# Kernel optimization log

Measured on AMD Instinct MI355X. Metric: run time of the kernel, lower is better.

The kernel has to match this reference:

```python
import jax, jax.numpy as jnp
import numpy as np

N, F, H, L, O, E = 20000, 128, 128, 4, 64, 640000
NEG_SLOPE = 0.2  # PyG GATConv default


def setup_inputs() -> dict:
    key = jax.random.key(0)
    ks = jax.random.split(key, 8)
    x = jax.random.normal(ks[0], (N, F), dtype=jnp.float32)
    edge_index = jax.random.randint(ks[1], (2, E), 0, N, dtype=jnp.int64)
    sc = 1.0 / np.sqrt(F)
    Ws = jax.random.normal(ks[2], (L, F, H), dtype=jnp.float32) * sc
    att_src = jax.random.normal(ks[3], (L, H), dtype=jnp.float32) * sc
    att_dst = jax.random.normal(ks[4], (L, H), dtype=jnp.float32) * sc
    biases = jnp.zeros((L, H), dtype=jnp.float32)
    W_out = jax.random.normal(ks[5], (H, O), dtype=jnp.float32) * (1.0 / np.sqrt(H))
    b_out = jnp.zeros((O,), dtype=jnp.float32)
    return {"x": x, "edge_index": edge_index, "Ws": Ws, "att_src": att_src,
            "att_dst": att_dst, "biases": biases, "W_out": W_out, "b_out": b_out}


def _gat_conv(h, src, dst, W, a_s, a_d, b):
    # h: [N, F_in]; single-head GATConv (PyG semantics)
    z = h @ W                                   # [N, H]
    alpha_s = z @ a_s                           # [N]
    alpha_d = z @ a_d                           # [N]
    logits = jax.nn.leaky_relu(alpha_s[src] + alpha_d[dst], negative_slope=NEG_SLOPE)  # [E']
    # segment-softmax over edges grouped by destination node
    m = jax.ops.segment_max(logits, dst, num_segments=N)
    p = jnp.exp(logits - m[dst])
    s = jax.ops.segment_sum(p, dst, num_segments=N)
    alpha = p / (s[dst] + 1e-16)                # [E']
    out = jax.ops.segment_sum(alpha[:, None] * z[src], dst, num_segments=N)  # [N, H]
    return out + b


def reference(x, edge_index, Ws, att_src, att_dst, biases, W_out, b_out):
    # add self-loops once (PyG GATConv default add_self_loops=True)
    loop = jnp.arange(N, dtype=edge_index.dtype)
    src = jnp.concatenate([edge_index[0], loop])
    dst = jnp.concatenate([edge_index[1], loop])
    h = x
    for l in range(L):
        h = _gat_conv(h, src, dst, Ws[l], att_src[l], att_dst[l], biases[l])
        h = jax.nn.relu(h)  # Dropout is identity at eval
    return h @ W_out + b_out  # [N, O]
```

## Files before the change

### kernel.cpp

```cpp
#include <hip/hip_runtime.h>

#define NN 20000
#define FF 128
#define HH 128
#define LL 4
#define OO 64
#define EE 640000
#define NEG 0.2f
#define NB ((NN + 255) / 256)
#define NTILES (NN / 16)

typedef short bf16x8 __attribute__((ext_vector_type(8)));
typedef float f32x4 __attribute__((ext_vector_type(4)));

__device__ inline ushort f2bf(float f) {
    uint u = __float_as_uint(f);
    return (ushort)((u + 0x7fffu + ((u >> 16) & 1u)) >> 16);
}


__global__ void k_init_counters(int* __restrict__ counters) {
    int i = blockIdx.x * 256 + threadIdx.x;
    if (i < NN) counters[i] = 1;
}

__global__ void k_hist(const int* __restrict__ dst, int* __restrict__ counters) {
    int e = blockIdx.x * 256 + threadIdx.x;
    if (e < EE) atomicAdd(&counters[dst[e]], 1);
}

__global__ void k_partial(const int* __restrict__ counters, int* __restrict__ partials) {
    __shared__ int ws[4];
    int t = threadIdx.x;
    int i = blockIdx.x * 256 + t;
    int c = (i < NN) ? counters[i] : 0;
    #pragma unroll
    for (int off = 32; off; off >>= 1) c += __shfl_xor(c, off);
    if ((t & 63) == 0) ws[t >> 6] = c;
    __syncthreads();
    if (t == 0) partials[blockIdx.x] = ws[0] + ws[1] + ws[2] + ws[3];
}

__global__ void k_scan_small(const int* __restrict__ partials, int* __restrict__ offsets) {
    __shared__ int sp[128];
    int t = threadIdx.x;
    int v = (t < NB) ? partials[t] : 0;
    sp[t] = v;
    __syncthreads();
    for (int off = 1; off < 128; off <<= 1) {
        int u = (t >= off) ? sp[t - off] : 0;
        __syncthreads();
        sp[t] += u;
        __syncthreads();
    }
    if (t < NB) offsets[t] = sp[t] - v;
}

__global__ void k_apply(const int* __restrict__ counters, const int* __restrict__ offsets,
                        int* __restrict__ row_off, int* __restrict__ cursor,
                        int* __restrict__ src_sorted) {
    __shared__ int sc[256];
    int t = threadIdx.x;
    int i = blockIdx.x * 256 + t;
    int c = (i < NN) ? counters[i] : 0;
    sc[t] = c;
    __syncthreads();
    for (int off = 1; off < 256; off <<= 1) {
        int u = (t >= off) ? sc[t - off] : 0;
        __syncthreads();
        sc[t] += u;
        __syncthreads();
    }
    int incl = sc[t];
    int base = offsets[blockIdx.x];
    if (i < NN) {
        int excl = base + incl - c;
        row_off[i] = excl;
        cursor[i] = excl + 1;
        src_sorted[excl] = i;
        if (i == NN - 1) row_off[NN] = base + incl;
    }
}

__global__ void k_scatter(const int* __restrict__ src, const int* __restrict__ dst,
                          int* __restrict__ cursor, int* __restrict__ src_sorted) {
    int e = blockIdx.x * 256 + threadIdx.x;
    if (e < EE) {
        int p = atomicAdd(&cursor[dst[e]], 1);
        src_sorted[p] = src[e];
    }
}


__global__ void k_convw(const float* __restrict__ Ws, const float* __restrict__ Wout,
                        ushort* __restrict__ wh, ushort* __restrict__ wl) {
    int idx = blockIdx.x * 256 + threadIdx.x;
    const int per_l = HH * 128;
    float v;
    if (idx < LL * per_l) {
        int l = idx / per_l, rem = idx % per_l;
        int n = rem >> 7, k = rem & 127;
        v = Ws[(size_t)l * 128 * HH + (size_t)k * HH + n];
    } else {
        int j = idx - LL * per_l;
        if (j >= OO * 128) return;
        int n = j >> 7, k = j & 127;
        v = Wout[(size_t)k * OO + n];
    }
    ushort h = f2bf(v);
    float hf = __uint_as_float((uint)h << 16);
    wh[idx] = h;
    wl[idx] = f2bf(v - hf);
}


__global__ void k_wa(const float* __restrict__ Ws, const float* __restrict__ attS,
                     const float* __restrict__ attD, float* __restrict__ wa) {
    int t = blockIdx.x * 256 + threadIdx.x;
    if (t >= LL * 256) return;
    int l = t >> 8, rem = t & 255, which = rem >> 7, k = rem & 127;
    const float* wrow = Ws + (size_t)l * 128 * HH + (size_t)k * HH;
    const float* av = (which ? attD : attS) + l * HH;
    float s = 0.f;
    #pragma unroll 4
    for (int n = 0; n < HH; n++) s += wrow[n] * av[n];
    wa[l * 256 + which * 128 + k] = s;
}


__device__ inline void do_agg(const float* __restrict__ z, const float* __restrict__ as,
                              const float* __restrict__ ad, const int* __restrict__ row_off,
                              const int* __restrict__ srcs, const float* __restrict__ bias,
                              float (*h)[132], int node0, int wid, int l64) {
    int g = l64 >> 5, cl = l64 & 31;
    const float4* zb = (const float4*)z;
    #pragma unroll 1
    for (int i = 0; i < 4; i++) {
        int node = node0 + wid * 4 + i;
        int beg = row_off[node], end = row_off[node + 1];
        float adn = ad[node];
        float lself = as[node] + adn;
        float mx = (lself >= 0.f) ? lself : NEG * lself;

        float4 acc = make_float4(0.f, 0.f, 0.f, 0.f);
        float s = 0.f;
        for (int e = beg + g; e < end; e += 16) {
            int e1 = e + 2, e2 = e + 4, e3 = e + 6, e4 = e + 8, e5 = e + 10, e6 = e + 12, e7 = e + 14;
            int lim = end - 1;
            int i1 = min(e1, lim), i2 = min(e2, lim), i3 = min(e3, lim);
            int i4 = min(e4, lim), i5 = min(e5, lim), i6 = min(e6, lim), i7 = min(e7, lim);
            int s0 = srcs[e], s1 = srcs[i1], s2 = srcs[i2], s3 = srcs[i3];
            int s4 = srcs[i4], s5 = srcs[i5], s6 = srcs[i6], s7 = srcs[i7];
            float l0 = as[s0] + adn, l1 = as[s1] + adn, l2 = as[s2] + adn, l3 = as[s3] + adn;
            float l4 = as[s4] + adn, l5 = as[s5] + adn, l6 = as[s6] + adn, l7 = as[s7] + adn;
            l0 = (l0 >= 0.f) ? l0 : NEG * l0;  l1 = (l1 >= 0.f) ? l1 : NEG * l1;
            l2 = (l2 >= 0.f) ? l2 : NEG * l2;  l3 = (l3 >= 0.f) ? l3 : NEG * l3;
            l4 = (l4 >= 0.f) ? l4 : NEG * l4;  l5 = (l5 >= 0.f) ? l5 : NEG * l5;
            l6 = (l6 >= 0.f) ? l6 : NEG * l6;  l7 = (l7 >= 0.f) ? l7 : NEG * l7;
            float4 z0 = zb[(size_t)s0 * 32 + cl];
            float4 z1 = zb[(size_t)s1 * 32 + cl];
            float4 z2 = zb[(size_t)s2 * 32 + cl];
            float4 z3 = zb[(size_t)s3 * 32 + cl];
            float4 z4 = zb[(size_t)s4 * 32 + cl];
            float4 z5 = zb[(size_t)s5 * 32 + cl];
            float4 z6 = zb[(size_t)s6 * 32 + cl];
            float4 z7 = zb[(size_t)s7 * 32 + cl];
            float p0 = __expf(l0 - mx);
            float p1 = (e1 < end) ? __expf(l1 - mx) : 0.f;
            float p2 = (e2 < end) ? __expf(l2 - mx) : 0.f;
            float p3 = (e3 < end) ? __expf(l3 - mx) : 0.f;
            float p4 = (e4 < end) ? __expf(l4 - mx) : 0.f;
            float p5 = (e5 < end) ? __expf(l5 - mx) : 0.f;
            float p6 = (e6 < end) ? __expf(l6 - mx) : 0.f;
            float p7 = (e7 < end) ? __expf(l7 - mx) : 0.f;
            s += ((p0 + p1) + (p2 + p3)) + ((p4 + p5) + (p6 + p7));
            acc.x += (p0 * z0.x + p1 * z1.x + p2 * z2.x + p3 * z3.x)
                   + (p4 * z4.x + p5 * z5.x + p6 * z6.x + p7 * z7.x);
            acc.y += (p0 * z0.y + p1 * z1.y + p2 * z2.y + p3 * z3.y)
                   + (p4 * z4.y + p5 * z5.y + p6 * z6.y + p7 * z7.y);
            acc.z += (p0 * z0.z + p1 * z1.z + p2 * z2.z + p3 * z3.z)
                   + (p4 * z4.z + p5 * z5.z + p6 * z6.z + p7 * z7.z);
            acc.w += (p0 * z0.w + p1 * z1.w + p2 * z2.w + p3 * z3.w)
                   + (p4 * z4.w + p5 * z5.w + p6 * z6.w + p7 * z7.w);
        }
        acc.x += __shfl_xor(acc.x, 32);
        acc.y += __shfl_xor(acc.y, 32);
        acc.z += __shfl_xor(acc.z, 32);
        acc.w += __shfl_xor(acc.w, 32);
        s     += __shfl_xor(s, 32);
        if (g == 0) {
            float inv = 1.f / (s + 1e-16f);
            float4 b = ((const float4*)bias)[cl];
            int lrow = wid * 4 + i;
            h[lrow][cl * 4 + 0] = fmaxf(acc.x * inv + b.x, 0.f);
            h[lrow][cl * 4 + 1] = fmaxf(acc.y * inv + b.y, 0.f);
            h[lrow][cl * 4 + 2] = fmaxf(acc.z * inv + b.z, 0.f);
            h[lrow][cl * 4 + 3] = fmaxf(acc.w * inv + b.w, 0.f);
        }
    }
}

template <int NCOL, bool BIAS, bool ALPHAS>
__device__ inline void do_gemm(const float (*h)[132], const ushort* __restrict__ wh,
                               const ushort* __restrict__ wl, const float* __restrict__ bias,
                               float* __restrict__ C, const float* __restrict__ wa,
                               float* __restrict__ as_o, float* __restrict__ ad_o,
                               int row0, int wid, int l64) {
    constexpr int CT = NCOL / 32;
    if (CT < 4 && wid >= CT) return;
    int ct = wid;
    int lr = l64 & 15, lg = l64 >> 4;
    int col0 = ct * 32;

    f32x4 af0[4], af1[4];
    #pragma unroll
    for (int s = 0; s < 4; s++) {
        af0[s] = *(const f32x4*)&h[lr][s * 32 + lg * 8];
        af1[s] = *(const f32x4*)&h[lr][s * 32 + lg * 8 + 4];
    }
    bf16x8 ah[4], al[4];
    #pragma unroll
    for (int s = 0; s < 4; s++) {
        #pragma unroll
        for (int j = 0; j < 8; j++) {
            float v = (j < 4) ? af0[s][j] : af1[s][j - 4];
            ushort hb = f2bf(v);
            float hf = __uint_as_float((uint)hb << 16);
            ah[s][j] = (short)hb;
            al[s][j] = (short)f2bf(v - hf);
        }
    }

    f32x4 acc[2] = {{0.f, 0.f, 0.f, 0.f}, {0.f, 0.f, 0.f, 0.f}};
    #pragma unroll
    for (int s = 0; s < 4; s++) {
        #pragma unroll
        for (int nt = 0; nt < 2; nt++) {
            int woff = (col0 + nt * 16 + lr) * 128 + s * 32 + lg * 8;
            bf16x8 bh = *(const bf16x8*)(wh + woff);
            bf16x8 bl = *(const bf16x8*)(wl + woff);
            acc[nt] = __builtin_amdgcn_mfma_f32_16x16x32_bf16(ah[s], bh, acc[nt], 0, 0, 0);
            acc[nt] = __builtin_amdgcn_mfma_f32_16x16x32_bf16(ah[s], bl, acc[nt], 0, 0, 0);
            acc[nt] = __builtin_amdgcn_mfma_f32_16x16x32_bf16(al[s], bh, acc[nt], 0, 0, 0);
        }
    }

    int orow = lg * 4;
    #pragma unroll
    for (int nt = 0; nt < 2; nt++) {
        #pragma unroll
        for (int r = 0; r < 4; r++) {
            float v = acc[nt][r];
            if (BIAS) v += bias[col0 + nt * 16 + lr];
            C[(size_t)(row0 + orow + r) * NCOL + col0 + nt * 16 + lr] = v;
        }
    }

    if constexpr (ALPHAS) {
        if (ct == 0) {
            float ps = 0.f, pd = 0.f;
            #pragma unroll
            for (int s = 0; s < 4; s++) {
                #pragma unroll
                for (int j = 0; j < 8; j++) {
                    float v = (j < 4) ? af0[s][j] : af1[s][j - 4];
                    int k = s * 32 + lg * 8 + j;
                    ps += v * wa[k];
                    pd += v * wa[128 + k];
                }
            }
            ps += __shfl_xor(ps, 16);  pd += __shfl_xor(pd, 16);
            ps += __shfl_xor(ps, 32);  pd += __shfl_xor(pd, 32);
            if (lg == 0) {
                as_o[row0 + lr] = ps;
                ad_o[row0 + lr] = pd;
            }
        }
    }
}


__global__ __launch_bounds__(256)
void k_layer0(const float* __restrict__ x, const ushort* __restrict__ wh,
              const ushort* __restrict__ wl, const float* __restrict__ wa,
              float* __restrict__ z, float* __restrict__ as_o, float* __restrict__ ad_o) {
    __shared__ float h[16][132];
    int t = threadIdx.x, wid = t >> 6, l64 = t & 63;
    int row0 = blockIdx.x * 16;
    for (int i = t; i < 16 * 32; i += 256) {
        int r = i >> 5, c4 = (i & 31) << 2;
        *(float4*)&h[r][c4] = *(const float4*)&x[(size_t)(row0 + r) * 128 + c4];
    }
    __syncthreads();
    do_gemm<HH, false, true>(h, wh, wl, nullptr, z, wa, as_o, ad_o, row0, wid, l64);
}

template <int NCOL, bool BIAS, bool ALPHAS>
__global__ __launch_bounds__(256)
void k_layer(const float* __restrict__ zin, const float* __restrict__ asi,
             const float* __restrict__ adi, const int* __restrict__ row_off,
             const int* __restrict__ srcs, const float* __restrict__ abias,
             const ushort* __restrict__ wh, const ushort* __restrict__ wl,
             const float* __restrict__ cbias, const float* __restrict__ wa,
             float* __restrict__ zout, float* __restrict__ as_o, float* __restrict__ ad_o) {
    __shared__ float h[16][132];
    int t = threadIdx.x, wid = t >> 6, l64 = t & 63;
    int row0 = blockIdx.x * 16;
    do_agg(zin, asi, adi, row_off, srcs, abias, h, row0, wid, l64);
    __syncthreads();
    do_gemm<NCOL, BIAS, ALPHAS>(h, wh, wl, cbias, zout, wa, as_o, ad_o, row0, wid, l64);
}


extern "C" void kernel_launch(void* const* d_in, const int* in_sizes, int n_in,
                              void* d_out, int out_size, void* d_ws, size_t ws_size,
                              hipStream_t stream) {
    const float* x      = (const float*)d_in[0];
    const int*   ei     = (const int*)d_in[1];
    const float* Ws     = (const float*)d_in[2];
    const float* attS   = (const float*)d_in[3];
    const float* attD   = (const float*)d_in[4];
    const float* biases = (const float*)d_in[5];
    const float* W_out  = (const float*)d_in[6];
    const float* b_out  = (const float*)d_in[7];
    float* out = (float*)d_out;

    const int* srcp = ei;
    const int* dstp = ei + EE;

    char* w = (char*)d_ws;
    auto take = [&](size_t bytes) {
        char* p = w;
        w += (bytes + 15) & ~(size_t)15;
        return p;
    };
    float*  za         = (float*)take((size_t)NN * HH * 4);
    float*  zbv        = (float*)take((size_t)NN * HH * 4);
    float*  asa        = (float*)take((size_t)NN * 4);
    float*  ada        = (float*)take((size_t)NN * 4);
    float*  asb        = (float*)take((size_t)NN * 4);
    float*  adb        = (float*)take((size_t)NN * 4);
    int*    counters   = (int*)take((size_t)NN * 4);
    int*    row_off    = (int*)take((size_t)(NN + 1) * 4);
    int*    cursor     = (int*)take((size_t)NN * 4);
    int*    src_sorted = (int*)take((size_t)(EE + NN) * 4);
    int*    partials   = (int*)take((size_t)NB * 4);
    int*    offsets    = (int*)take((size_t)NB * 4);
    const int WTOT = LL * HH * 128 + OO * 128;
    ushort* whbuf      = (ushort*)take((size_t)WTOT * 2);
    ushort* wlbuf      = (ushort*)take((size_t)WTOT * 2);
    float*  wabuf      = (float*)take((size_t)LL * 256 * 4);

    k_init_counters<<<(NN + 255) / 256, 256, 0, stream>>>(counters);
    k_hist<<<(EE + 255) / 256, 256, 0, stream>>>(dstp, counters);
    k_partial<<<NB, 256, 0, stream>>>(counters, partials);
    k_scan_small<<<1, 128, 0, stream>>>(partials, offsets);
    k_apply<<<NB, 256, 0, stream>>>(counters, offsets, row_off, cursor, src_sorted);
    k_scatter<<<(EE + 255) / 256, 256, 0, stream>>>(srcp, dstp, cursor, src_sorted);
    k_convw<<<(WTOT + 255) / 256, 256, 0, stream>>>(Ws, W_out, whbuf, wlbuf);
    k_wa<<<(LL * 256 + 255) / 256, 256, 0, stream>>>(Ws, attS, attD, wabuf);

    k_layer0<<<NTILES, 256, 0, stream>>>(x, whbuf, wlbuf, wabuf, za, asa, ada);

    k_layer<HH, false, true><<<NTILES, 256, 0, stream>>>(
        za, asa, ada, row_off, src_sorted, biases + 0 * HH,
        whbuf + (size_t)1 * HH * 128, wlbuf + (size_t)1 * HH * 128,
        nullptr, wabuf + 1 * 256, zbv, asb, adb);
    k_layer<HH, false, true><<<NTILES, 256, 0, stream>>>(
        zbv, asb, adb, row_off, src_sorted, biases + 1 * HH,
        whbuf + (size_t)2 * HH * 128, wlbuf + (size_t)2 * HH * 128,
        nullptr, wabuf + 2 * 256, za, asa, ada);
    k_layer<HH, false, true><<<NTILES, 256, 0, stream>>>(
        za, asa, ada, row_off, src_sorted, biases + 2 * HH,
        whbuf + (size_t)3 * HH * 128, wlbuf + (size_t)3 * HH * 128,
        nullptr, wabuf + 3 * 256, zbv, asb, adb);

    k_layer<OO, true, false><<<NTILES, 256, 0, stream>>>(
        zbv, asb, adb, row_off, src_sorted, biases + 3 * HH,
        whbuf + (size_t)LL * HH * 128, wlbuf + (size_t)LL * HH * 128,
        b_out, nullptr, out, nullptr, nullptr);
}
```

Measured before the change: 377.2 us.

## Pack attention scalars into padded z rows and double threads per block

Stores alpha_src and alpha_dst in the first two floats of each node's z row, padded to a 132-float stride with features at offset 4. This lets the gather read the logit scalar from the same row as the feature vector instead of from separate arrays. Blocks grow to 512 threads: each wave aggregates 2 nodes instead of 4, and the GEMM gives each wave one 16-column tile instead of two. The padding makes the z buffers slightly larger, and the scalar at offset 0 may sit in a different cache line from the features, so the locality gain is not assured.

```diff
diff --git a/kernel.cpp b/kernel.cpp
--- a/kernel.cpp
+++ b/kernel.cpp
@@ -9,6 +9,7 @@
 #define NEG 0.2f
 #define NB ((NN + 255) / 256)
 #define NTILES (NN / 16)
+#define ZS 132
 
 typedef short bf16x8 __attribute__((ext_vector_type(8)));
 typedef float f32x4 __attribute__((ext_vector_type(4)));
@@ -128,18 +129,17 @@
 }
 
 
-__device__ inline void do_agg(const float* __restrict__ z, const float* __restrict__ as,
-                              const float* __restrict__ ad, const int* __restrict__ row_off,
+__device__ inline void do_agg(const float* __restrict__ zin, const int* __restrict__ row_off,
                               const int* __restrict__ srcs, const float* __restrict__ bias,
                               float (*h)[132], int node0, int wid, int l64) {
     int g = l64 >> 5, cl = l64 & 31;
-    const float4* zb = (const float4*)z;
+    const float4* zb = (const float4*)zin;
     #pragma unroll 1
-    for (int i = 0; i < 4; i++) {
-        int node = node0 + wid * 4 + i;
+    for (int i = 0; i < 2; i++) {
+        int node = node0 + wid * 2 + i;
         int beg = row_off[node], end = row_off[node + 1];
-        float adn = ad[node];
-        float lself = as[node] + adn;
+        float adn = zin[(size_t)node * ZS + 1];
+        float lself = zin[(size_t)node * ZS] + adn;
         float mx = (lself >= 0.f) ? lself : NEG * lself;
 
         float4 acc = make_float4(0.f, 0.f, 0.f, 0.f);
@@ -151,20 +151,22 @@
             int i4 = min(e4, lim), i5 = min(e5, lim), i6 = min(e6, lim), i7 = min(e7, lim);
             int s0 = srcs[e], s1 = srcs[i1], s2 = srcs[i2], s3 = srcs[i3];
             int s4 = srcs[i4], s5 = srcs[i5], s6 = srcs[i6], s7 = srcs[i7];
-            float l0 = as[s0] + adn, l1 = as[s1] + adn, l2 = as[s2] + adn, l3 = as[s3] + adn;
-            float l4 = as[s4] + adn, l5 = as[s5] + adn, l6 = as[s6] + adn, l7 = as[s7] + adn;
+            float l0 = zin[(size_t)s0 * ZS] + adn, l1 = zin[(size_t)s1 * ZS] + adn;
+            float l2 = zin[(size_t)s2 * ZS] + adn, l3 = zin[(size_t)s3 * ZS] + adn;
+            float l4 = zin[(size_t)s4 * ZS] + adn, l5 = zin[(size_t)s5 * ZS] + adn;
+            float l6 = zin[(size_t)s6 * ZS] + adn, l7 = zin[(size_t)s7 * ZS] + adn;
             l0 = (l0 >= 0.f) ? l0 : NEG * l0;  l1 = (l1 >= 0.f) ? l1 : NEG * l1;
             l2 = (l2 >= 0.f) ? l2 : NEG * l2;  l3 = (l3 >= 0.f) ? l3 : NEG * l3;
             l4 = (l4 >= 0.f) ? l4 : NEG * l4;  l5 = (l5 >= 0.f) ? l5 : NEG * l5;
             l6 = (l6 >= 0.f) ? l6 : NEG * l6;  l7 = (l7 >= 0.f) ? l7 : NEG * l7;
-            float4 z0 = zb[(size_t)s0 * 32 + cl];
-            float4 z1 = zb[(size_t)s1 * 32 + cl];
-            float4 z2 = zb[(size_t)s2 * 32 + cl];
-            float4 z3 = zb[(size_t)s3 * 32 + cl];
-            float4 z4 = zb[(size_t)s4 * 32 + cl];
-            float4 z5 = zb[(size_t)s5 * 32 + cl];
-            float4 z6 = zb[(size_t)s6 * 32 + cl];
-            float4 z7 = zb[(size_t)s7 * 32 + cl];
+            float4 z0 = zb[(size_t)s0 * 33 + 1 + cl];
+            float4 z1 = zb[(size_t)s1 * 33 + 1 + cl];
+            float4 z2 = zb[(size_t)s2 * 33 + 1 + cl];
+            float4 z3 = zb[(size_t)s3 * 33 + 1 + cl];
+            float4 z4 = zb[(size_t)s4 * 33 + 1 + cl];
+            float4 z5 = zb[(size_t)s5 * 33 + 1 + cl];
+            float4 z6 = zb[(size_t)s6 * 33 + 1 + cl];
+            float4 z7 = zb[(size_t)s7 * 33 + 1 + cl];
             float p0 = __expf(l0 - mx);
             float p1 = (e1 < end) ? __expf(l1 - mx) : 0.f;
             float p2 = (e2 < end) ? __expf(l2 - mx) : 0.f;
@@ -191,7 +193,7 @@
         if (g == 0) {
             float inv = 1.f / (s + 1e-16f);
             float4 b = ((const float4*)bias)[cl];
-            int lrow = wid * 4 + i;
+            int lrow = wid * 2 + i;
             h[lrow][cl * 4 + 0] = fmaxf(acc.x * inv + b.x, 0.f);
             h[lrow][cl * 4 + 1] = fmaxf(acc.y * inv + b.y, 0.f);
             h[lrow][cl * 4 + 2] = fmaxf(acc.z * inv + b.z, 0.f);
@@ -200,17 +202,15 @@
     }
 }
 
-template <int NCOL, bool BIAS, bool ALPHAS>
+template <int NCOL, bool BIAS, bool ALPHAS, bool PACKED>
 __device__ inline void do_gemm(const float (*h)[132], const ushort* __restrict__ wh,
                                const ushort* __restrict__ wl, const float* __restrict__ bias,
                                float* __restrict__ C, const float* __restrict__ wa,
-                               float* __restrict__ as_o, float* __restrict__ ad_o,
                                int row0, int wid, int l64) {
-    constexpr int CT = NCOL / 32;
-    if (CT < 4 && wid >= CT) return;
-    int ct = wid;
+    constexpr int CT = NCOL / 16;
+    if (wid >= CT) return;
     int lr = l64 & 15, lg = l64 >> 4;
-    int col0 = ct * 32;
+    int col0 = wid * 16;
 
     f32x4 af0[4], af1[4];
     #pragma unroll
@@ -231,33 +231,30 @@
         }
     }
 
-    f32x4 acc[2] = {{0.f, 0.f, 0.f, 0.f}, {0.f, 0.f, 0.f, 0.f}};
+    f32x4 acc = {0.f, 0.f, 0.f, 0.f};
     #pragma unroll
     for (int s = 0; s < 4; s++) {
-        #pragma unroll
-        for (int nt = 0; nt < 2; nt++) {
-            int woff = (col0 + nt * 16 + lr) * 128 + s * 32 + lg * 8;
-            bf16x8 bh = *(const bf16x8*)(wh + woff);
-            bf16x8 bl = *(const bf16x8*)(wl + woff);
-            acc[nt] = __builtin_amdgcn_mfma_f32_16x16x32_bf16(ah[s], bh, acc[nt], 0, 0, 0);
-            acc[nt] = __builtin_amdgcn_mfma_f32_16x16x32_bf16(ah[s], bl, acc[nt], 0, 0, 0);
-            acc[nt] = __builtin_amdgcn_mfma_f32_16x16x32_bf16(al[s], bh, acc[nt], 0, 0, 0);
-        }
+        int woff = (col0 + lr) * 128 + s * 32 + lg * 8;
+        bf16x8 bh = *(const bf16x8*)(wh + woff);
+        bf16x8 bl = *(const bf16x8*)(wl + woff);
+        acc = __builtin_amdgcn_mfma_f32_16x16x32_bf16(ah[s], bh, acc, 0, 0, 0);
+        acc = __builtin_amdgcn_mfma_f32_16x16x32_bf16(ah[s], bl, acc, 0, 0, 0);
+        acc = __builtin_amdgcn_mfma_f32_16x16x32_bf16(al[s], bh, acc, 0, 0, 0);
     }
 
     int orow = lg * 4;
     #pragma unroll
-    for (int nt = 0; nt < 2; nt++) {
-        #pragma unroll
-        for (int r = 0; r < 4; r++) {
-            float v = acc[nt][r];
-            if (BIAS) v += bias[col0 + nt * 16 + lr];
-            C[(size_t)(row0 + orow + r) * NCOL + col0 + nt * 16 + lr] = v;
-        }
+    for (int r = 0; r < 4; r++) {
+        float v = acc[r];
+        if (BIAS) v += bias[col0 + lr];
+        if (PACKED)
+            C[(size_t)(row0 + orow + r) * ZS + 4 + col0 + lr] = v;
+        else
+            C[(size_t)(row0 + orow + r) * NCOL + col0 + lr] = v;
     }
 
     if constexpr (ALPHAS) {
-        if (ct == 0) {
+        if (wid == 0) {
             float ps = 0.f, pd = 0.f;
             #pragma unroll
             for (int s = 0; s < 4; s++) {
@@ -272,43 +269,42 @@
             ps += __shfl_xor(ps, 16);  pd += __shfl_xor(pd, 16);
             ps += __shfl_xor(ps, 32);  pd += __shfl_xor(pd, 32);
             if (lg == 0) {
-                as_o[row0 + lr] = ps;
-                ad_o[row0 + lr] = pd;
+                C[(size_t)(row0 + lr) * ZS + 0] = ps;
+                C[(size_t)(row0 + lr) * ZS + 1] = pd;
             }
         }
     }
 }
 
 
-__global__ __launch_bounds__(256)
+__global__ __launch_bounds__(512)
 void k_layer0(const float* __restrict__ x, const ushort* __restrict__ wh,
               const ushort* __restrict__ wl, const float* __restrict__ wa,
-              float* __restrict__ z, float* __restrict__ as_o, float* __restrict__ ad_o) {
+              float* __restrict__ z) {
     __shared__ float h[16][132];
     int t = threadIdx.x, wid = t >> 6, l64 = t & 63;
     int row0 = blockIdx.x * 16;
-    for (int i = t; i < 16 * 32; i += 256) {
-        int r = i >> 5, c4 = (i & 31) << 2;
+    {
+        int r = t >> 5, c4 = (t & 31) << 2;
         *(float4*)&h[r][c4] = *(const float4*)&x[(size_t)(row0 + r) * 128 + c4];
     }
     __syncthreads();
-    do_gemm<HH, false, true>(h, wh, wl, nullptr, z, wa, as_o, ad_o, row0, wid, l64);
-}
-
-template <int NCOL, bool BIAS, bool ALPHAS>
-__global__ __launch_bounds__(256)
-void k_layer(const float* __restrict__ zin, const float* __restrict__ asi,
-             const float* __restrict__ adi, const int* __restrict__ row_off,
+    do_gemm<HH, false, true, true>(h, wh, wl, nullptr, z, wa, row0, wid, l64);
+}
+
+template <int NCOL, bool BIAS, bool ALPHAS, bool PACKED>
+__global__ __launch_bounds__(512)
+void k_layer(const float* __restrict__ zin, const int* __restrict__ row_off,
              const int* __restrict__ srcs, const float* __restrict__ abias,
              const ushort* __restrict__ wh, const ushort* __restrict__ wl,
              const float* __restrict__ cbias, const float* __restrict__ wa,
-             float* __restrict__ zout, float* __restrict__ as_o, float* __restrict__ ad_o) {
+             float* __restrict__ zout) {
     __shared__ float h[16][132];
     int t = threadIdx.x, wid = t >> 6, l64 = t & 63;
     int row0 = blockIdx.x * 16;
-    do_agg(zin, asi, adi, row_off, srcs, abias, h, row0, wid, l64);
-    __syncthreads();
-    do_gemm<NCOL, BIAS, ALPHAS>(h, wh, wl, cbias, zout, wa, as_o, ad_o, row0, wid, l64);
+    do_agg(zin, row_off, srcs, abias, h, row0, wid, l64);
+    __syncthreads();
+    do_gemm<NCOL, BIAS, ALPHAS, PACKED>(h, wh, wl, cbias, zout, wa, row0, wid, l64);
 }
 
 
@@ -334,12 +330,8 @@
         w += (bytes + 15) & ~(size_t)15;
         return p;
     };
-    float*  za         = (float*)take((size_t)NN * HH * 4);
-    float*  zbv        = (float*)take((size_t)NN * HH * 4);
-    float*  asa        = (float*)take((size_t)NN * 4);
-    float*  ada        = (float*)take((size_t)NN * 4);
-    float*  asb        = (float*)take((size_t)NN * 4);
-    float*  adb        = (float*)take((size_t)NN * 4);
+    float*  za         = (float*)take((size_t)NN * ZS * 4);
+    float*  zbv        = (float*)take((size_t)NN * ZS * 4);
     int*    counters   = (int*)take((size_t)NN * 4);
     int*    row_off    = (int*)take((size_t)(NN + 1) * 4);
     int*    cursor     = (int*)take((size_t)NN * 4);
@@ -360,23 +352,23 @@
     k_convw<<<(WTOT + 255) / 256, 256, 0, stream>>>(Ws, W_out, whbuf, wlbuf);
     k_wa<<<(LL * 256 + 255) / 256, 256, 0, stream>>>(Ws, attS, attD, wabuf);
 
-    k_layer0<<<NTILES, 256, 0, stream>>>(x, whbuf, wlbuf, wabuf, za, asa, ada);
-
-    k_layer<HH, false, true><<<NTILES, 256, 0, stream>>>(
-        za, asa, ada, row_off, src_sorted, biases + 0 * HH,
+    k_layer0<<<NTILES, 512, 0, stream>>>(x, whbuf, wlbuf, wabuf, za);
+
+    k_layer<HH, false, true, true><<<NTILES, 512, 0, stream>>>(
+        za, row_off, src_sorted, biases + 0 * HH,
         whbuf + (size_t)1 * HH * 128, wlbuf + (size_t)1 * HH * 128,
-        nullptr, wabuf + 1 * 256, zbv, asb, adb);
-    k_layer<HH, false, true><<<NTILES, 256, 0, stream>>>(
-        zbv, asb, adb, row_off, src_sorted, biases + 1 * HH,
+        nullptr, wabuf + 1 * 256, zbv);
+    k_layer<HH, false, true, true><<<NTILES, 512, 0, stream>>>(
+        zbv, row_off, src_sorted, biases + 1 * HH,
         whbuf + (size_t)2 * HH * 128, wlbuf + (size_t)2 * HH * 128,
-        nullptr, wabuf + 2 * 256, za, asa, ada);
-    k_layer<HH, false, true><<<NTILES, 256, 0, stream>>>(
-        za, asa, ada, row_off, src_sorted, biases + 2 * HH,
+        nullptr, wabuf + 2 * 256, za);
+    k_layer<HH, false, true, true><<<NTILES, 512, 0, stream>>>(
+        za, row_off, src_sorted, biases + 2 * HH,
         whbuf + (size_t)3 * HH * 128, wlbuf + (size_t)3 * HH * 128,
-        nullptr, wabuf + 3 * 256, zbv, asb, adb);
-
-    k_layer<OO, true, false><<<NTILES, 256, 0, stream>>>(
-        zbv, asb, adb, row_off, src_sorted, biases + 3 * HH,
+        nullptr, wabuf + 3 * 256, zbv);
+
+    k_layer<OO, true, false, false><<<NTILES, 512, 0, stream>>>(
+        zbv, row_off, src_sorted, biases + 3 * HH,
         whbuf + (size_t)LL * HH * 128, wlbuf + (size_t)LL * HH * 128,
-        b_out, nullptr, out, nullptr, nullptr);
-}
+        b_out, nullptr, out);
+}
```

Result: faster. 361.0 us (-4.3%).

## Use one wavefront per node in fused GAT layers with larger blocks

Applied to the files above, without the earlier changes.

Each 16-node tile block now launches 16 wavefronts (1024 threads), with each wave aggregating a single destination node instead of four nodes serially. The GEMM stage splits output columns into 16-wide slices, one per wave, so up to 8 waves do MFMA work instead of 4. Layer 0 uses 512 threads so each thread loads exactly one float4 of the input tile. The aim is more memory-level parallelism for the gather-heavy aggregation. The cost is larger blocks, a register cap of 1024 threads per block, and idle waves during the GEMM phase.

```diff
diff --git a/kernel.cpp b/kernel.cpp
--- a/kernel.cpp
+++ b/kernel.cpp
@@ -128,77 +128,73 @@
 }
 
 
-__device__ inline void do_agg(const float* __restrict__ z, const float* __restrict__ as,
-                              const float* __restrict__ ad, const int* __restrict__ row_off,
-                              const int* __restrict__ srcs, const float* __restrict__ bias,
-                              float (*h)[132], int node0, int wid, int l64) {
+__device__ inline void do_agg1(const float* __restrict__ z, const float* __restrict__ asv,
+                               const float* __restrict__ adv, const int* __restrict__ row_off,
+                               const int* __restrict__ srcs, const float* __restrict__ bias,
+                               float (*h)[132], int node, int lrow, int l64) {
     int g = l64 >> 5, cl = l64 & 31;
     const float4* zb = (const float4*)z;
-    #pragma unroll 1
-    for (int i = 0; i < 4; i++) {
-        int node = node0 + wid * 4 + i;
-        int beg = row_off[node], end = row_off[node + 1];
-        float adn = ad[node];
-        float lself = as[node] + adn;
-        float mx = (lself >= 0.f) ? lself : NEG * lself;
-
-        float4 acc = make_float4(0.f, 0.f, 0.f, 0.f);
-        float s = 0.f;
-        for (int e = beg + g; e < end; e += 16) {
-            int e1 = e + 2, e2 = e + 4, e3 = e + 6, e4 = e + 8, e5 = e + 10, e6 = e + 12, e7 = e + 14;
-            int lim = end - 1;
-            int i1 = min(e1, lim), i2 = min(e2, lim), i3 = min(e3, lim);
-            int i4 = min(e4, lim), i5 = min(e5, lim), i6 = min(e6, lim), i7 = min(e7, lim);
-            int s0 = srcs[e], s1 = srcs[i1], s2 = srcs[i2], s3 = srcs[i3];
-            int s4 = srcs[i4], s5 = srcs[i5], s6 = srcs[i6], s7 = srcs[i7];
-            float l0 = as[s0] + adn, l1 = as[s1] + adn, l2 = as[s2] + adn, l3 = as[s3] + adn;
-            float l4 = as[s4] + adn, l5 = as[s5] + adn, l6 = as[s6] + adn, l7 = as[s7] + adn;
-            l0 = (l0 >= 0.f) ? l0 : NEG * l0;  l1 = (l1 >= 0.f) ? l1 : NEG * l1;
-            l2 = (l2 >= 0.f) ? l2 : NEG * l2;  l3 = (l3 >= 0.f) ? l3 : NEG * l3;
-            l4 = (l4 >= 0.f) ? l4 : NEG * l4;  l5 = (l5 >= 0.f) ? l5 : NEG * l5;
-            l6 = (l6 >= 0.f) ? l6 : NEG * l6;  l7 = (l7 >= 0.f) ? l7 : NEG * l7;
-            float4 z0 = zb[(size_t)s0 * 32 + cl];
-            float4 z1 = zb[(size_t)s1 * 32 + cl];
-            float4 z2 = zb[(size_t)s2 * 32 + cl];
-            float4 z3 = zb[(size_t)s3 * 32 + cl];
-            float4 z4 = zb[(size_t)s4 * 32 + cl];
-            float4 z5 = zb[(size_t)s5 * 32 + cl];
-            float4 z6 = zb[(size_t)s6 * 32 + cl];
-            float4 z7 = zb[(size_t)s7 * 32 + cl];
-            float p0 = __expf(l0 - mx);
-            float p1 = (e1 < end) ? __expf(l1 - mx) : 0.f;
-            float p2 = (e2 < end) ? __expf(l2 - mx) : 0.f;
-            float p3 = (e3 < end) ? __expf(l3 - mx) : 0.f;
-            float p4 = (e4 < end) ? __expf(l4 - mx) : 0.f;
-            float p5 = (e5 < end) ? __expf(l5 - mx) : 0.f;
-            float p6 = (e6 < end) ? __expf(l6 - mx) : 0.f;
-            float p7 = (e7 < end) ? __expf(l7 - mx) : 0.f;
-            s += ((p0 + p1) + (p2 + p3)) + ((p4 + p5) + (p6 + p7));
-            acc.x += (p0 * z0.x + p1 * z1.x + p2 * z2.x + p3 * z3.x)
-                   + (p4 * z4.x + p5 * z5.x + p6 * z6.x + p7 * z7.x);
-            acc.y += (p0 * z0.y + p1 * z1.y + p2 * z2.y + p3 * z3.y)
-                   + (p4 * z4.y + p5 * z5.y + p6 * z6.y + p7 * z7.y);
-            acc.z += (p0 * z0.z + p1 * z1.z + p2 * z2.z + p3 * z3.z)
-                   + (p4 * z4.z + p5 * z5.z + p6 * z6.z + p7 * z7.z);
-            acc.w += (p0 * z0.w + p1 * z1.w + p2 * z2.w + p3 * z3.w)
-                   + (p4 * z4.w + p5 * z5.w + p6 * z6.w + p7 * z7.w);
-        }
-        acc.x += __shfl_xor(acc.x, 32);
-        acc.y += __shfl_xor(acc.y, 32);
-        acc.z += __shfl_xor(acc.z, 32);
-        acc.w += __shfl_xor(acc.w, 32);
-        s     += __shfl_xor(s, 32);
-        if (g == 0) {
-            float inv = 1.f / (s + 1e-16f);
-            float4 b = ((const float4*)bias)[cl];
-            int lrow = wid * 4 + i;
-            h[lrow][cl * 4 + 0] = fmaxf(acc.x * inv + b.x, 0.f);
-            h[lrow][cl * 4 + 1] = fmaxf(acc.y * inv + b.y, 0.f);
-            h[lrow][cl * 4 + 2] = fmaxf(acc.z * inv + b.z, 0.f);
-            h[lrow][cl * 4 + 3] = fmaxf(acc.w * inv + b.w, 0.f);
-        }
-    }
-}
+    int beg = row_off[node], end = row_off[node + 1];
+    float adn = adv[node];
+    float lself = asv[node] + adn;
+    float mx = (lself >= 0.f) ? lself : NEG * lself;
+
+    float4 acc = make_float4(0.f, 0.f, 0.f, 0.f);
+    float s = 0.f;
+    for (int e = beg + g; e < end; e += 16) {
+        int e1 = e + 2, e2 = e + 4, e3 = e + 6, e4 = e + 8, e5 = e + 10, e6 = e + 12, e7 = e + 14;
+        int lim = end - 1;
+        int i1 = min(e1, lim), i2 = min(e2, lim), i3 = min(e3, lim);
+        int i4 = min(e4, lim), i5 = min(e5, lim), i6 = min(e6, lim), i7 = min(e7, lim);
+        int s0 = srcs[e], s1 = srcs[i1], s2 = srcs[i2], s3 = srcs[i3];
+        int s4 = srcs[i4], s5 = srcs[i5], s6 = srcs[i6], s7 = srcs[i7];
+        float l0 = asv[s0] + adn, l1 = asv[s1] + adn, l2 = asv[s2] + adn, l3 = asv[s3] + adn;
+        float l4 = asv[s4] + adn, l5 = asv[s5] + adn, l6 = asv[s6] + adn, l7 = asv[s7] + adn;
+        l0 = (l0 >= 0.f) ? l0 : NEG * l0;  l1 = (l1 >= 0.f) ? l1 : NEG * l1;
+        l2 = (l2 >= 0.f) ? l2 : NEG * l2;  l3 = (l3 >= 0.f) ? l3 : NEG * l3;
+        l4 = (l4 >= 0.f) ? l4 : NEG * l4;  l5 = (l5 >= 0.f) ? l5 : NEG * l5;
+        l6 = (l6 >= 0.f) ? l6 : NEG * l6;  l7 = (l7 >= 0.f) ? l7 : NEG * l7;
+        float4 z0 = zb[(size_t)s0 * 32 + cl];
+        float4 z1 = zb[(size_t)s1 * 32 + cl];
+        float4 z2 = zb[(size_t)s2 * 32 + cl];
+        float4 z3 = zb[(size_t)s3 * 32 + cl];
+        float4 z4 = zb[(size_t)s4 * 32 + cl];
+        float4 z5 = zb[(size_t)s5 * 32 + cl];
+        float4 z6 = zb[(size_t)s6 * 32 + cl];
+        float4 z7 = zb[(size_t)s7 * 32 + cl];
+        float p0 = __expf(l0 - mx);
+        float p1 = (e1 < end) ? __expf(l1 - mx) : 0.f;
+        float p2 = (e2 < end) ? __expf(l2 - mx) : 0.f;
+        float p3 = (e3 < end) ? __expf(l3 - mx) : 0.f;
+        float p4 = (e4 < end) ? __expf(l4 - mx) : 0.f;
+        float p5 = (e5 < end) ? __expf(l5 - mx) : 0.f;
+        float p6 = (e6 < end) ? __expf(l6 - mx) : 0.f;
+        float p7 = (e7 < end) ? __expf(l7 - mx) : 0.f;
+        s += ((p0 + p1) + (p2 + p3)) + ((p4 + p5) + (p6 + p7));
+        acc.x += (p0 * z0.x + p1 * z1.x + p2 * z2.x + p3 * z3.x)
+               + (p4 * z4.x + p5 * z5.x + p6 * z6.x + p7 * z7.x);
+        acc.y += (p0 * z0.y + p1 * z1.y + p2 * z2.y + p3 * z3.y)
+               + (p4 * z4.y + p5 * z5.y + p6 * z6.y + p7 * z7.y);
+        acc.z += (p0 * z0.z + p1 * z1.z + p2 * z2.z + p3 * z3.z)
+               + (p4 * z4.z + p5 * z5.z + p6 * z6.z + p7 * z7.z);
+        acc.w += (p0 * z0.w + p1 * z1.w + p2 * z2.w + p3 * z3.w)
+               + (p4 * z4.w + p5 * z5.w + p6 * z6.w + p7 * z7.w);
+    }
+    acc.x += __shfl_xor(acc.x, 32);
+    acc.y += __shfl_xor(acc.y, 32);
+    acc.z += __shfl_xor(acc.z, 32);
+    acc.w += __shfl_xor(acc.w, 32);
+    s     += __shfl_xor(s, 32);
+    if (g == 0) {
+        float inv = 1.f / (s + 1e-16f);
+        float4 b = ((const float4*)bias)[cl];
+        h[lrow][cl * 4 + 0] = fmaxf(acc.x * inv + b.x, 0.f);
+        h[lrow][cl * 4 + 1] = fmaxf(acc.y * inv + b.y, 0.f);
+        h[lrow][cl * 4 + 2] = fmaxf(acc.z * inv + b.z, 0.f);
+        h[lrow][cl * 4 + 3] = fmaxf(acc.w * inv + b.w, 0.f);
+    }
+}
+
 
 template <int NCOL, bool BIAS, bool ALPHAS>
 __device__ inline void do_gemm(const float (*h)[132], const ushort* __restrict__ wh,
@@ -206,11 +202,10 @@
                                float* __restrict__ C, const float* __restrict__ wa,
                                float* __restrict__ as_o, float* __restrict__ ad_o,
                                int row0, int wid, int l64) {
-    constexpr int CT = NCOL / 32;
-    if (CT < 4 && wid >= CT) return;
-    int ct = wid;
+    constexpr int CT = NCOL / 16;
+    if (wid >= CT) return;
     int lr = l64 & 15, lg = l64 >> 4;
-    int col0 = ct * 32;
+    int col0 = wid * 16;
 
     f32x4 af0[4], af1[4];
     #pragma unroll
@@ -231,33 +226,28 @@
         }
     }
 
-    f32x4 acc[2] = {{0.f, 0.f, 0.f, 0.f}, {0.f, 0.f, 0.f, 0.f}};
+    f32x4 acc = {0.f, 0.f, 0.f, 0.f};
     #pragma unroll
     for (int s = 0; s < 4; s++) {
-        #pragma unroll
-        for (int nt = 0; nt < 2; nt++) {
-            int woff = (col0 + nt * 16 + lr) * 128 + s * 32 + lg * 8;
-            bf16x8 bh = *(const bf16x8*)(wh + woff);
-            bf16x8 bl = *(const bf16x8*)(wl + woff);
-            acc[nt] = __builtin_amdgcn_mfma_f32_16x16x32_bf16(ah[s], bh, acc[nt], 0, 0, 0);
-            acc[nt] = __builtin_amdgcn_mfma_f32_16x16x32_bf16(ah[s], bl, acc[nt], 0, 0, 0);
-            acc[nt] = __builtin_amdgcn_mfma_f32_16x16x32_bf16(al[s], bh, acc[nt], 0, 0, 0);
-        }
+        int woff = (col0 + lr) * 128 + s * 32 + lg * 8;
+        bf16x8 bh = *(const bf16x8*)(wh + woff);
+        bf16x8 bl = *(const bf16x8*)(wl + woff);
+        acc = __builtin_amdgcn_mfma_f32_16x16x32_bf16(ah[s], bh, acc, 0, 0, 0);
+        acc = __builtin_amdgcn_mfma_f32_16x16x32_bf16(ah[s], bl, acc, 0, 0, 0);
+        acc = __builtin_amdgcn_mfma_f32_16x16x32_bf16(al[s], bh, acc, 0, 0, 0);
     }
 
     int orow = lg * 4;
-    #pragma unroll
-    for (int nt = 0; nt < 2; nt++) {
-        #pragma unroll
-        for (int r = 0; r < 4; r++) {
-            float v = acc[nt][r];
-            if (BIAS) v += bias[col0 + nt * 16 + lr];
-            C[(size_t)(row0 + orow + r) * NCOL + col0 + nt * 16 + lr] = v;
-        }
+    int c = col0 + lr;
+    #pragma unroll
+    for (int r = 0; r < 4; r++) {
+        float v = acc[r];
+        if (BIAS) v += bias[c];
+        C[(size_t)(row0 + orow + r) * NCOL + c] = v;
     }
 
     if constexpr (ALPHAS) {
-        if (ct == 0) {
+        if (wid == 0) {
             float ps = 0.f, pd = 0.f;
             #pragma unroll
             for (int s = 0; s < 4; s++) {
@@ -280,15 +270,15 @@
 }
 
 
-__global__ __launch_bounds__(256)
+__global__ __launch_bounds__(512)
 void k_layer0(const float* __restrict__ x, const ushort* __restrict__ wh,
               const ushort* __restrict__ wl, const float* __restrict__ wa,
               float* __restrict__ z, float* __restrict__ as_o, float* __restrict__ ad_o) {
     __shared__ float h[16][132];
     int t = threadIdx.x, wid = t >> 6, l64 = t & 63;
     int row0 = blockIdx.x * 16;
-    for (int i = t; i < 16 * 32; i += 256) {
-        int r = i >> 5, c4 = (i & 31) << 2;
+    {
+        int r = t >> 5, c4 = (t & 31) << 2;
         *(float4*)&h[r][c4] = *(const float4*)&x[(size_t)(row0 + r) * 128 + c4];
     }
     __syncthreads();
@@ -296,7 +286,7 @@
 }
 
 template <int NCOL, bool BIAS, bool ALPHAS>
-__global__ __launch_bounds__(256)
+__global__ __launch_bounds__(1024)
 void k_layer(const float* __restrict__ zin, const float* __restrict__ asi,
              const float* __restrict__ adi, const int* __restrict__ row_off,
              const int* __restrict__ srcs, const float* __restrict__ abias,
@@ -306,7 +296,7 @@
     __shared__ float h[16][132];
     int t = threadIdx.x, wid = t >> 6, l64 = t & 63;
     int row0 = blockIdx.x * 16;
-    do_agg(zin, asi, adi, row_off, srcs, abias, h, row0, wid, l64);
+    do_agg1(zin, asi, adi, row_off, srcs, abias, h, row0 + wid, wid, l64);
     __syncthreads();
     do_gemm<NCOL, BIAS, ALPHAS>(h, wh, wl, cbias, zout, wa, as_o, ad_o, row0, wid, l64);
 }
@@ -360,22 +350,22 @@
     k_convw<<<(WTOT + 255) / 256, 256, 0, stream>>>(Ws, W_out, whbuf, wlbuf);
     k_wa<<<(LL * 256 + 255) / 256, 256, 0, stream>>>(Ws, attS, attD, wabuf);
 
-    k_layer0<<<NTILES, 256, 0, stream>>>(x, whbuf, wlbuf, wabuf, za, asa, ada);
-
-    k_layer<HH, false, true><<<NTILES, 256, 0, stream>>>(
+    k_layer0<<<NTILES, 512, 0, stream>>>(x, whbuf, wlbuf, wabuf, za, asa, ada);
+
+    k_layer<HH, false, true><<<NTILES, 1024, 0, stream>>>(
         za, asa, ada, row_off, src_sorted, biases + 0 * HH,
         whbuf + (size_t)1 * HH * 128, wlbuf + (size_t)1 * HH * 128,
         nullptr, wabuf + 1 * 256, zbv, asb, adb);
-    k_layer<HH, false, true><<<NTILES, 256, 0, stream>>>(
+    k_layer<HH, false, true><<<NTILES, 1024, 0, stream>>>(
         zbv, asb, adb, row_off, src_sorted, biases + 1 * HH,
         whbuf + (size_t)2 * HH * 128, wlbuf + (size_t)2 * HH * 128,
         nullptr, wabuf + 2 * 256, za, asa, ada);
-    k_layer<HH, false, true><<<NTILES, 256, 0, stream>>>(
+    k_layer<HH, false, true><<<NTILES, 1024, 0, stream>>>(
         za, asa, ada, row_off, src_sorted, biases + 2 * HH,
         whbuf + (size_t)3 * HH * 128, wlbuf + (size_t)3 * HH * 128,
         nullptr, wabuf + 3 * 256, zbv, asb, adb);
 
-    k_layer<OO, true, false><<<NTILES, 256, 0, stream>>>(
+    k_layer<OO, true, false><<<NTILES, 1024, 0, stream>>>(
         zbv, asb, adb, row_off, src_sorted, biases + 3 * HH,
         whbuf + (size_t)LL * HH * 128, wlbuf + (size_t)LL * HH * 128,
         b_out, nullptr, out, nullptr, nullptr);
```

Result: no change. 377.2 us (-0.0%).
